# Kernel optimization log

Hardware: AMD Instinct MI355X
Metric: run time of the kernel (lower is better)

Reference implementation:

```python
import jax, jax.numpy as jnp
import numpy as np

N_NODES = 50000
N_EDGES = 800000
D = 128
N_RELS = 460  # 2 * num_rels
N_BASES = 32
SUBMAT = D // N_BASES  # 4
INV_TEMP = 0.1


def setup_inputs() -> dict:
    key = jax.random.key(0)
    ks = jax.random.split(key, 16)
    return {
        "h": jax.random.normal(ks[0], (N_NODES, D), jnp.float32),
        "first_prev": jax.random.normal(ks[1], (N_NODES, D), jnp.float32),
        "second_prev": jax.random.normal(ks[2], (N_NODES, D), jnp.float32),
        "time_diff": jax.random.uniform(ks[3], (N_NODES, 1), jnp.float32),
        "edge_src": jax.random.randint(ks[4], (N_EDGES,), 0, N_NODES, jnp.int32),
        "edge_dst": jax.random.randint(ks[5], (N_EDGES,), 0, N_NODES, jnp.int32),
        "edge_type": jax.random.randint(ks[6], (N_EDGES,), 0, N_RELS, jnp.int32),
        "edge_norm": jax.random.uniform(ks[7], (N_EDGES, 1), jnp.float32),
        "node_norm": jax.random.uniform(ks[8], (N_NODES, 1), jnp.float32),
        "W1": jax.random.normal(ks[9], (N_RELS, N_BASES * SUBMAT * SUBMAT), jnp.float32) * 0.05,
        "W2": jax.random.normal(ks[10], (N_RELS, N_BASES * SUBMAT * SUBMAT), jnp.float32) * 0.05,
        "loop_w1": jax.random.normal(ks[11], (D, D), jnp.float32) * 0.05,
        "loop_w2": jax.random.normal(ks[12], (D, D), jnp.float32) * 0.05,
        "time_w1": jax.random.normal(ks[13], (D, D), jnp.float32) * 0.05,
        "time_w2": jax.random.normal(ks[14], (D, D), jnp.float32) * 0.05,
    }


def _drgcn_layer(h, prev, time_diff, W, loop_w, time_w,
                 edge_src, edge_dst, edge_type, edge_norm, node_norm, activate):
    n = h.shape[0]
    # self-loop message (dropout is identity in eval)
    loop_msg = h @ loop_w                                     # [N, D]
    # block-diagonal per-edge message: gather relation blocks + batched small matmul
    w = W[edge_type].reshape(-1, N_BASES, SUBMAT, SUBMAT)     # [E, B, si, so]
    hs = h[edge_src].reshape(-1, N_BASES, SUBMAT)             # [E, B, si]
    msg = jnp.einsum('ebi,ebio->ebo', hs, w).reshape(-1, h.shape[1])  # [E, D]
    msg = msg * edge_norm                                     # per-edge norm
    agg = jax.ops.segment_sum(msg, edge_dst, num_segments=n)  # scatter-sum to dst
    agg = agg * node_norm                                     # apply_func node norm
    # time-decay residual + self-loop (bias=None in this config)
    out = agg + (prev @ time_w) * jnp.exp(-time_diff * INV_TEMP) + loop_msg
    if activate:
        out = jax.nn.relu(out)
    return out


def reference(h, first_prev, second_prev, time_diff,
              edge_src, edge_dst, edge_type, edge_norm, node_norm,
              W1, W2, loop_w1, loop_w2, time_w1, time_w2):
    h1 = _drgcn_layer(h, first_prev, time_diff, W1, loop_w1, time_w1,
                      edge_src, edge_dst, edge_type, edge_norm, node_norm, activate=False)
    h2 = _drgcn_layer(h1, second_prev, time_diff, W2, loop_w2, time_w2,
                      edge_src, edge_dst, edge_type, edge_norm, node_norm, activate=True)
    return (h1, h2)
```

## Files before the change

### kernel.cpp

```cpp
#include <hip/hip_runtime.h>

#define NN 50000
#define NE 800000
#define DD 128
#define NPAD 50176
#define NBLK_SCAN 196

typedef __attribute__((ext_vector_type(8))) short short8;
typedef __attribute__((ext_vector_type(4))) float f32x4;

static __device__ __forceinline__ float b2f_lo(unsigned u) {
    return __builtin_bit_cast(float, u << 16);
}
static __device__ __forceinline__ float b2f_hi(unsigned u) {
    return __builtin_bit_cast(float, u & 0xffff0000u);
}
static __device__ __forceinline__ unsigned short f2b(float f) {
    unsigned u = __builtin_bit_cast(unsigned, f);
    u += 0x7FFFu + ((u >> 16) & 1u);
    return (unsigned short)(u >> 16);
}
static __device__ __forceinline__ ushort4 f2b4(float4 v) {
    ushort4 u;
    u.x = f2b(v.x); u.y = f2b(v.y); u.z = f2b(v.z); u.w = f2b(v.w);
    return u;
}

__global__ __launch_bounds__(256) void k_hist(
    const int* __restrict__ edst, int* __restrict__ cnt)
{
    const int e = blockIdx.x * 256 + threadIdx.x;
    atomicAdd(&cnt[edst[e]], 1);
}

__global__ __launch_bounds__(256) void k_scan_a(
    const int* __restrict__ cnt, int* __restrict__ bsum)
{
    __shared__ int s[256];
    const int t = threadIdx.x;
    s[t] = cnt[blockIdx.x * 256 + t];
    __syncthreads();
    for (int d = 128; d > 0; d >>= 1) {
        if (t < d) s[t] += s[t + d];
        __syncthreads();
    }
    if (t == 0) bsum[blockIdx.x] = s[0];
}

__global__ __launch_bounds__(256) void k_scan_b(int* __restrict__ bsum)
{
    __shared__ int s[256];
    const int t = threadIdx.x;
    s[t] = (t < NBLK_SCAN) ? bsum[t] : 0;
    __syncthreads();
    for (int d = 1; d < 256; d <<= 1) {
        int v = (t >= d) ? s[t - d] : 0;
        __syncthreads();
        s[t] += v;
        __syncthreads();
    }
    bsum[t] = (t == 0) ? 0 : s[t - 1];
}

__global__ __launch_bounds__(256) void k_scan_c(
    const int* __restrict__ cnt, const int* __restrict__ bsum,
    int* __restrict__ off, int* __restrict__ cur)
{
    __shared__ int s[256];
    const int t = threadIdx.x;
    const int i = blockIdx.x * 256 + t;
    const int c = cnt[i];
    s[t] = c;
    __syncthreads();
    for (int d = 1; d < 256; d <<= 1) {
        int v = (t >= d) ? s[t - d] : 0;
        __syncthreads();
        s[t] += v;
        __syncthreads();
    }
    const int ex = bsum[blockIdx.x] + s[t] - c;
    off[i] = ex;
    cur[i] = ex;
}

__global__ __launch_bounds__(256) void k_scatter(
    const int* __restrict__ esrc, const int* __restrict__ edst,
    const int* __restrict__ etyp, const float* __restrict__ enorm,
    int* __restrict__ cur, int4* __restrict__ sedge)
{
    const int e = blockIdx.x * 256 + threadIdx.x;
    const int d = edst[e];
    const int pos = atomicAdd(&cur[d], 1);
    sedge[pos] = make_int4(esrc[e], etyp[e],
                           __builtin_bit_cast(int, enorm[e]), d);
}

#define PREP_X_BLOCKS 6250
#define PREP_W_BLOCKS 460
#define PREP_BLOCKS   (PREP_X_BLOCKS + PREP_W_BLOCKS + 32)

__global__ __launch_bounds__(256) void k_prep(
    const float* __restrict__ x, const float* __restrict__ fprev,
    const float* __restrict__ sprev, const float* __restrict__ tdiff,
    unsigned short* __restrict__ X1, unsigned short* __restrict__ X2,
    const float* __restrict__ W1, const float* __restrict__ W2,
    unsigned short* __restrict__ W1b, unsigned short* __restrict__ W2b,
    const float* __restrict__ lw1, const float* __restrict__ tw1,
    const float* __restrict__ lw2, const float* __restrict__ tw2,
    unsigned short* __restrict__ Wp1, unsigned short* __restrict__ Wp2)
{
    const int gb = blockIdx.x;
    const int t  = threadIdx.x;
    if (gb < PREP_X_BLOCKS) {
        const int idx = gb * 256 + t;
        const int n = idx >> 5, j = (idx & 31) * 4;
        const float dk = __expf(-tdiff[n] * 0.1f);
        const float4 a = *(const float4*)(x     + (size_t)n * 128 + j);
        float4 b = *(const float4*)(fprev + (size_t)n * 128 + j);
        float4 c = *(const float4*)(sprev + (size_t)n * 128 + j);
        b.x *= dk; b.y *= dk; b.z *= dk; b.w *= dk;
        c.x *= dk; c.y *= dk; c.z *= dk; c.w *= dk;
        *(ushort4*)(X1 + (size_t)n * 256 + j)       = f2b4(a);
        *(ushort4*)(X1 + (size_t)n * 256 + 128 + j) = f2b4(b);
        *(ushort4*)(X2 + (size_t)n * 256 + 128 + j) = f2b4(c);
    } else if (gb < PREP_X_BLOCKS + PREP_W_BLOCKS) {
        const int i = ((gb - PREP_X_BLOCKS) * 256 + t) * 4;
        if (i < 460 * 512) {
            *(ushort4*)(W1b + i) = f2b4(*(const float4*)(W1 + i));
        } else {
            const int k = i - 460 * 512;
            *(ushort4*)(W2b + k) = f2b4(*(const float4*)(W2 + k));
        }
    } else {
        const int g = (gb - PREP_X_BLOCKS - PREP_W_BLOCKS) * 256 + t;
        const int c = g & 4095;
        const float* lw = (g < 4096) ? lw1 : lw2;
        const float* tw = (g < 4096) ? tw1 : tw2;
        unsigned short* Wp = (g < 4096) ? Wp1 : Wp2;
        const int ct = c >> 9, ks = (c >> 6) & 7, lane = c & 63;
        const int col = ct * 16 + (lane & 15);
        unsigned short* o = Wp + (size_t)c * 8;
        #pragma unroll
        for (int i = 0; i < 8; ++i) {
            const int k = ks * 32 + (lane >> 4) * 8 + i;
            const float v = (k < 128) ? lw[(size_t)k * 128 + col]
                                      : tw[(size_t)(k - 128) * 128 + col];
            o[i] = f2b(v);
        }
    }
}

__device__ __forceinline__ void agg_edge(
    const unsigned short* __restrict__ x,
    const unsigned short* __restrict__ Wb,
    const int4* __restrict__ sedge, int i,
    int woff, int l, float4& acc)
{
    const int4 e = sedge[i];
    const int src = __builtin_amdgcn_readfirstlane(e.x);
    const int typ = __builtin_amdgcn_readfirstlane(e.y);
    const float nr = __builtin_bit_cast(float, __builtin_amdgcn_readfirstlane(e.z));
    const unsigned hw = ((const unsigned*)(x + (size_t)src * 256))[l];
    const uint4 wv = *(const uint4*)(Wb + (size_t)typ * 512 + woff);
    const float h0 = b2f_lo(hw) * nr;
    const float h1 = b2f_hi(hw) * nr;
    acc.x += h0 * b2f_lo(wv.x) + h1 * b2f_lo(wv.z);
    acc.y += h0 * b2f_hi(wv.x) + h1 * b2f_hi(wv.z);
    acc.z += h0 * b2f_lo(wv.y) + h1 * b2f_lo(wv.w);
    acc.w += h0 * b2f_hi(wv.y) + h1 * b2f_hi(wv.w);
}

__global__ __launch_bounds__(256) void k_agg2(
    const unsigned short* __restrict__ x,
    const int4*  __restrict__ sedge,
    const int*   __restrict__ off,
    const unsigned short* __restrict__ Wb,
    const float* __restrict__ nnorm,
    float*       __restrict__ agg)
{
    const int l = threadIdx.x & 63;
    const int n = blockIdx.x * 4 + (threadIdx.x >> 6);
    const int beg = off[n], end = off[n + 1];
    const int woff = (l >> 1) * 16 + (l & 1) * 8;

    float4 a0 = {0,0,0,0}, a1 = {0,0,0,0}, a2 = {0,0,0,0}, a3 = {0,0,0,0};

    int i = beg;
    for (; i + 4 <= end; i += 4) {
        agg_edge(x, Wb, sedge, i,     woff, l, a0);
        agg_edge(x, Wb, sedge, i + 1, woff, l, a1);
        agg_edge(x, Wb, sedge, i + 2, woff, l, a2);
        agg_edge(x, Wb, sedge, i + 3, woff, l, a3);
    }
    for (; i < end; ++i) agg_edge(x, Wb, sedge, i, woff, l, a0);

    float4 s;
    s.x = (a0.x + a1.x) + (a2.x + a3.x);
    s.y = (a0.y + a1.y) + (a2.y + a3.y);
    s.z = (a0.z + a1.z) + (a2.z + a3.z);
    s.w = (a0.w + a1.w) + (a2.w + a3.w);
    s.x += __shfl_xor(s.x, 1);
    s.y += __shfl_xor(s.y, 1);
    s.z += __shfl_xor(s.z, 1);
    s.w += __shfl_xor(s.w, 1);

    const float nn = nnorm[n];
    const float e0 = (l & 1) ? s.z : s.x;
    const float e1 = (l & 1) ? s.w : s.y;
    float2* outp = (float2*)(agg + (size_t)n * DD + (l >> 1) * 4 + (l & 1) * 2);
    *outp = make_float2(e0 * nn, e1 * nn);
}

template<int ACT, int WRITE_NEXT>
__global__ __launch_bounds__(256) void combine_mfma(
    const float* __restrict__ agg,
    const unsigned short* __restrict__ X,
    const unsigned short* __restrict__ Wp,
    float* __restrict__ out,
    unsigned short* __restrict__ Xnext)
{
    const int t = threadIdx.x;
    const int l = t & 63;
    const int w = t >> 6;
    const int wr = w >> 1, wc = w & 1;
    const int l15 = l & 15, lhi = l >> 4;
    const int rowbase = blockIdx.x * 64 + wr * 32;

    f32x4 acc[2][4] = {};

    const int ar0 = min(rowbase + l15, NN - 1);
    const int ar1 = min(rowbase + 16 + l15, NN - 1);
    const unsigned short* a0p = X + (size_t)ar0 * 256 + lhi * 8;
    const unsigned short* a1p = X + (size_t)ar1 * 256 + lhi * 8;
    const unsigned short* bp  = Wp + (size_t)(wc * 4) * 8 * 512 + (size_t)l * 8;

    #pragma unroll
    for (int ks = 0; ks < 8; ++ks) {
        const short8 a0 = *(const short8*)(a0p + ks * 32);
        const short8 a1 = *(const short8*)(a1p + ks * 32);
        #pragma unroll
        for (int ct = 0; ct < 4; ++ct) {
            const short8 b = *(const short8*)(bp + (size_t)(ct * 8 + ks) * 512);
            acc[0][ct] = __builtin_amdgcn_mfma_f32_16x16x32_bf16(a0, b, acc[0][ct], 0, 0, 0);
            acc[1][ct] = __builtin_amdgcn_mfma_f32_16x16x32_bf16(a1, b, acc[1][ct], 0, 0, 0);
        }
    }

    __shared__ float cs[64][132];
    #pragma unroll
    for (int rg = 0; rg < 2; ++rg)
        #pragma unroll
        for (int ct = 0; ct < 4; ++ct)
            #pragma unroll
            for (int q = 0; q < 4; ++q)
                cs[wr * 32 + rg * 16 + lhi * 4 + q][wc * 64 + ct * 16 + l15]
                    = acc[rg][ct][q];
    __syncthreads();

    const int r = t >> 2;
    const int s = t & 3;
    const int grow = blockIdx.x * 64 + r;
    if (grow < NN) {
        const float* aggr = agg + (size_t)grow * DD;
        float*       outr = out + (size_t)grow * DD;
        #pragma unroll
        for (int i = 0; i < 8; ++i) {
            const int c = s * 4 + i * 16;
            const float4 a  = *(const float4*)(aggr + c);
            const float4 cc = *(const float4*)&cs[r][c];
            float4 v = make_float4(a.x + cc.x, a.y + cc.y, a.z + cc.z, a.w + cc.w);
            if (ACT) {
                v.x = fmaxf(v.x, 0.f); v.y = fmaxf(v.y, 0.f);
                v.z = fmaxf(v.z, 0.f); v.w = fmaxf(v.w, 0.f);
            }
            *(float4*)(outr + c) = v;
            if (WRITE_NEXT)
                *(ushort4*)(Xnext + (size_t)grow * 256 + c) = f2b4(v);
        }
    }
}

__device__ __forceinline__ float pick4(float4 v, int o) {
    float a = (o & 1) ? v.y : v.x;
    float b = (o & 1) ? v.w : v.z;
    return (o & 2) ? b : a;
}

__global__ __launch_bounds__(256) void k_agg_t2(
    const float* __restrict__ x, const int4* __restrict__ sedge,
    const int* __restrict__ off, const float* __restrict__ W,
    float* __restrict__ agg)
{
    const int lane = threadIdx.x & 63;
    const int n    = blockIdx.x * 4 + (threadIdx.x >> 6);
    const int beg = off[n], end = off[n + 1];
    float4 acca = make_float4(0.f, 0.f, 0.f, 0.f);
    float4 accb = make_float4(0.f, 0.f, 0.f, 0.f);
    for (int i = beg; i < end; ++i) {
        const int4 e = sedge[i];
        const float nr = __builtin_bit_cast(float, e.z);
        const float* wr = W + (size_t)e.y * 512 + 4 * lane;
        const float4 wa = *(const float4*)wr;
        const float4 wb = *(const float4*)(wr + 256);
        const float* hr = x + (size_t)e.x * DD;
        const float ha = hr[lane] * nr;
        const float hb = hr[64 + lane] * nr;
        acca.x += ha * wa.x; acca.y += ha * wa.y; acca.z += ha * wa.z; acca.w += ha * wa.w;
        accb.x += hb * wb.x; accb.y += hb * wb.y; accb.z += hb * wb.z; accb.w += hb * wb.w;
    }
    #pragma unroll
    for (int d = 1; d <= 2; d <<= 1) {
        acca.x += __shfl_xor(acca.x, d); acca.y += __shfl_xor(acca.y, d);
        acca.z += __shfl_xor(acca.z, d); acca.w += __shfl_xor(acca.w, d);
        accb.x += __shfl_xor(accb.x, d); accb.y += __shfl_xor(accb.y, d);
        accb.z += __shfl_xor(accb.z, d); accb.w += __shfl_xor(accb.w, d);
    }
    const int o = lane & 3;
    agg[(size_t)n * DD + lane]      = pick4(acca, o);
    agg[(size_t)n * DD + 64 + lane] = pick4(accb, o);
}

__global__ __launch_bounds__(256) void edge_msg(
    const float* __restrict__ x, const int* __restrict__ esrc,
    const int* __restrict__ edst, const int* __restrict__ etyp,
    const float* __restrict__ enorm, const float* __restrict__ W,
    float* __restrict__ agg)
{
    const int t  = threadIdx.x;
    const int le = t >> 7;
    const int j  = t & 127;
    const int e  = blockIdx.x * 2 + le;
    __shared__ float sh[2][DD];
    sh[le][j] = x[(size_t)esrc[e] * DD + j];
    __syncthreads();
    const int b = j >> 2, o = j & 3;
    const float* wr = W + (size_t)etyp[e] * 512 + b * 16 + o;
    const float4 hv = *(const float4*)&sh[le][b * 4];
    float m = hv.x * wr[0] + hv.y * wr[4] + hv.z * wr[8] + hv.w * wr[12];
    m *= enorm[e];
    atomicAdd(&agg[(size_t)edst[e] * DD + j], m);
}

template<int ACT>
__global__ __launch_bounds__(256) void combine(
    float* __restrict__ out, const float* __restrict__ x,
    const float* __restrict__ prev, const float* __restrict__ tdiff,
    const float* __restrict__ nnorm, const float* __restrict__ lw,
    const float* __restrict__ tw)
{
    const int t = threadIdx.x;
    const int j = t & 127;
    const int r = t >> 7;
    const int base = blockIdx.x * 8;
    __shared__ float sh[8][DD];
    __shared__ float sp[8][DD];
    #pragma unroll
    for (int q = 0; q < 4; ++q) {
        const int m = q * 2 + r;
        const int n = base + m;
        const float decay = __expf(-tdiff[n] * 0.1f);
        sh[m][j] = x[(size_t)n * DD + j];
        sp[m][j] = prev[(size_t)n * DD + j] * decay;
    }
    __syncthreads();
    float acc[4] = {0.f, 0.f, 0.f, 0.f};
    for (int k = 0; k < DD; k += 4) {
        float wl[4], wt[4];
        #pragma unroll
        for (int kk = 0; kk < 4; ++kk) {
            wl[kk] = lw[(size_t)(k + kk) * DD + j];
            wt[kk] = tw[(size_t)(k + kk) * DD + j];
        }
        #pragma unroll
        for (int q = 0; q < 4; ++q) {
            const int m = q * 2 + r;
            const float4 a = *(const float4*)&sh[m][k];
            const float4 p = *(const float4*)&sp[m][k];
            acc[q] += a.x * wl[0] + a.y * wl[1] + a.z * wl[2] + a.w * wl[3]
                    + p.x * wt[0] + p.y * wt[1] + p.z * wt[2] + p.w * wt[3];
        }
    }
    #pragma unroll
    for (int q = 0; q < 4; ++q) {
        const int m = q * 2 + r;
        const int n = base + m;
        float v = out[(size_t)n * DD + j] * nnorm[n] + acc[q];
        if (ACT) v = fmaxf(v, 0.f);
        out[(size_t)n * DD + j] = v;
    }
}

extern "C" void kernel_launch(void* const* d_in, const int* in_sizes, int n_in,
                              void* d_out, int out_size, void* d_ws, size_t ws_size,
                              hipStream_t stream) {
    const float* h     = (const float*)d_in[0];
    const float* fprev = (const float*)d_in[1];
    const float* sprev = (const float*)d_in[2];
    const float* tdiff = (const float*)d_in[3];
    const int*   esrc  = (const int*)d_in[4];
    const int*   edst  = (const int*)d_in[5];
    const int*   etyp  = (const int*)d_in[6];
    const float* enorm = (const float*)d_in[7];
    const float* nnorm = (const float*)d_in[8];
    const float* W1    = (const float*)d_in[9];
    const float* W2    = (const float*)d_in[10];
    const float* lw1   = (const float*)d_in[11];
    const float* lw2   = (const float*)d_in[12];
    const float* tw1   = (const float*)d_in[13];
    const float* tw2   = (const float*)d_in[14];

    float* h1 = (float*)d_out;
    float* h2 = h1 + (size_t)NN * DD;
    const size_t layer_bytes = (size_t)NN * DD * sizeof(float);

    char* wsp = (char*)d_ws;
    int*   cnt   = (int*)wsp;  wsp += (size_t)NPAD * 4;
    int*   off   = (int*)wsp;  wsp += (size_t)NPAD * 4;
    int*   cur   = (int*)wsp;  wsp += (size_t)NPAD * 4;
    int*   bsum  = (int*)wsp;  wsp += 256 * 4;
    int4*  sedge = (int4*)wsp; wsp += (size_t)NE * 16;
    const size_t ws_sorted = (size_t)(wsp - (char*)d_ws);
    unsigned short* X1   = (unsigned short*)wsp; wsp += (size_t)NN * 256 * 2;
    unsigned short* X2   = (unsigned short*)wsp; wsp += (size_t)NN * 256 * 2;
    unsigned short* Wc1p = (unsigned short*)wsp; wsp += 4096 * 8 * 2;
    unsigned short* Wc2p = (unsigned short*)wsp; wsp += 4096 * 8 * 2;
    unsigned short* W1b  = (unsigned short*)wsp; wsp += (size_t)460 * 512 * 2;
    unsigned short* W2b  = (unsigned short*)wsp; wsp += (size_t)460 * 512 * 2;
    const size_t ws_full = (size_t)(wsp - (char*)d_ws);

    const int grid_mm = (NN + 63) / 64;

    if (ws_size >= ws_full) {
        hipMemsetAsync(cnt, 0, (size_t)NPAD * 4, stream);
        k_hist   <<<NE / 256, 256, 0, stream>>>(edst, cnt);
        k_scan_a <<<NBLK_SCAN, 256, 0, stream>>>(cnt, bsum);
        k_scan_b <<<1, 256, 0, stream>>>(bsum);
        k_scan_c <<<NBLK_SCAN, 256, 0, stream>>>(cnt, bsum, off, cur);
        k_scatter<<<NE / 256, 256, 0, stream>>>(esrc, edst, etyp, enorm, cur, sedge);
        k_prep<<<PREP_BLOCKS, 256, 0, stream>>>(
            h, fprev, sprev, tdiff, X1, X2,
            W1, W2, W1b, W2b, lw1, tw1, lw2, tw2, Wc1p, Wc2p);
        k_agg2<<<NN / 4, 256, 0, stream>>>(X1, sedge, off, W1b, nnorm, h1);
        combine_mfma<0, 1><<<grid_mm, 256, 0, stream>>>(h1, X1, Wc1p, h1, X2);
        k_agg2<<<NN / 4, 256, 0, stream>>>(X2, sedge, off, W2b, nnorm, h2);
        combine_mfma<1, 0><<<grid_mm, 256, 0, stream>>>(h2, X2, Wc2p, h2, nullptr);
    } else if (ws_size >= ws_sorted) {
        hipMemsetAsync(cnt, 0, (size_t)NPAD * 4, stream);
        k_hist   <<<NE / 256, 256, 0, stream>>>(edst, cnt);
        k_scan_a <<<NBLK_SCAN, 256, 0, stream>>>(cnt, bsum);
        k_scan_b <<<1, 256, 0, stream>>>(bsum);
        k_scan_c <<<NBLK_SCAN, 256, 0, stream>>>(cnt, bsum, off, cur);
        k_scatter<<<NE / 256, 256, 0, stream>>>(esrc, edst, etyp, enorm, cur, sedge);
        k_agg_t2<<<NN / 4, 256, 0, stream>>>(h, sedge, off, W1, h1);
        combine<0><<<NN / 8, 256, 0, stream>>>(h1, h, fprev, tdiff, nnorm, lw1, tw1);
        k_agg_t2<<<NN / 4, 256, 0, stream>>>(h1, sedge, off, W2, h2);
        combine<1><<<NN / 8, 256, 0, stream>>>(h2, h1, sprev, tdiff, nnorm, lw2, tw2);
    } else {
        hipMemsetAsync(h1, 0, layer_bytes, stream);
        edge_msg<<<NE / 2, 256, 0, stream>>>(h, esrc, edst, etyp, enorm, W1, h1);
        combine<0><<<NN / 8, 256, 0, stream>>>(h1, h, fprev, tdiff, nnorm, lw1, tw1);
        hipMemsetAsync(h2, 0, layer_bytes, stream);
        edge_msg<<<NE / 2, 256, 0, stream>>>(h1, esrc, edst, etyp, enorm, W2, h2);
        combine<1><<<NN / 8, 256, 0, stream>>>(h2, h1, sprev, tdiff, nnorm, lw2, tw2);
    }
}
```

Measured before the change: 423.1 us.

## Fuse CSR build and prep into one cooperative kernel with grid syncs

Replaces the memset, histogram, three scan kernels, scatter and prep launches with a single cooperative kernel of 1024 blocks that separates the phases with grid-wide syncs. The aim is to remove per-launch overhead and gaps between the small kernels that build the destination-sorted edge list. In exchange it adds grid.sync barriers, and 1024 persistent blocks may leave parts of the device idle during the serial scan phases. If the cooperative launch fails, the code falls back to the original sequence of kernels.

```diff
diff --git a/kernel.cpp b/kernel.cpp
--- a/kernel.cpp
+++ b/kernel.cpp
@@ -1,10 +1,14 @@
 #include <hip/hip_runtime.h>
+#include <hip/hip_cooperative_groups.h>
+
+namespace cg = cooperative_groups;
 
 #define NN 50000
 #define NE 800000
 #define DD 128
 #define NPAD 50176
 #define NBLK_SCAN 196
+#define BUILD_BLOCKS 1024
 
 typedef __attribute__((ext_vector_type(8))) short short8;
 typedef __attribute__((ext_vector_type(4))) float f32x4;
@@ -24,6 +28,115 @@
     ushort4 u;
     u.x = f2b(v.x); u.y = f2b(v.y); u.z = f2b(v.z); u.w = f2b(v.w);
     return u;
+}
+
+struct BuildArgs {
+    const int* esrc; const int* edst; const int* etyp; const float* enorm;
+    int* cnt; int* off; int* cur; int* bsum; int4* sedge;
+    const float* x; const float* fprev; const float* sprev; const float* tdiff;
+    unsigned short* X1; unsigned short* X2;
+    const float* W1; const float* W2;
+    unsigned short* W1b; unsigned short* W2b;
+    const float* lw1; const float* tw1; const float* lw2; const float* tw2;
+    unsigned short* Wp1; unsigned short* Wp2;
+};
+
+__global__ __launch_bounds__(256, 4) void k_build(BuildArgs a)
+{
+    cg::grid_group grid = cg::this_grid();
+    const int tid = blockIdx.x * 256 + threadIdx.x;
+    const int nth = gridDim.x * 256;
+
+    for (int i = tid; i < NPAD; i += nth) a.cnt[i] = 0;
+
+    for (int q = tid; q < NN * 32; q += nth) {
+        const int n = q >> 5, j = (q & 31) * 4;
+        const float dk = __expf(-a.tdiff[n] * 0.1f);
+        const float4 xa = *(const float4*)(a.x     + (size_t)n * 128 + j);
+        float4 b = *(const float4*)(a.fprev + (size_t)n * 128 + j);
+        float4 c = *(const float4*)(a.sprev + (size_t)n * 128 + j);
+        b.x *= dk; b.y *= dk; b.z *= dk; b.w *= dk;
+        c.x *= dk; c.y *= dk; c.z *= dk; c.w *= dk;
+        *(ushort4*)(a.X1 + (size_t)n * 256 + j)       = f2b4(xa);
+        *(ushort4*)(a.X1 + (size_t)n * 256 + 128 + j) = f2b4(b);
+        *(ushort4*)(a.X2 + (size_t)n * 256 + 128 + j) = f2b4(c);
+    }
+
+    for (int q = tid; q < 2 * 460 * 512 / 4; q += nth) {
+        const int i = q * 4;
+        if (i < 460 * 512)
+            *(ushort4*)(a.W1b + i) = f2b4(*(const float4*)(a.W1 + i));
+        else {
+            const int k = i - 460 * 512;
+            *(ushort4*)(a.W2b + k) = f2b4(*(const float4*)(a.W2 + k));
+        }
+    }
+
+    for (int g = tid; g < 8192; g += nth) {
+        const int c = g & 4095;
+        const float* lw = (g < 4096) ? a.lw1 : a.lw2;
+        const float* tw = (g < 4096) ? a.tw1 : a.tw2;
+        unsigned short* Wp = (g < 4096) ? a.Wp1 : a.Wp2;
+        const int ct = c >> 9, ks = (c >> 6) & 7, lane = c & 63;
+        const int col = ct * 16 + (lane & 15);
+        unsigned short* o = Wp + (size_t)c * 8;
+        #pragma unroll
+        for (int i = 0; i < 8; ++i) {
+            const int k = ks * 32 + (lane >> 4) * 8 + i;
+            const float v = (k < 128) ? lw[(size_t)k * 128 + col]
+                                      : tw[(size_t)(k - 128) * 128 + col];
+            o[i] = f2b(v);
+        }
+    }
+    grid.sync();
+
+    for (int e = tid; e < NE; e += nth) atomicAdd(&a.cnt[a.edst[e]], 1);
+    grid.sync();
+
+    __shared__ int s[256];
+    if (blockIdx.x < NBLK_SCAN) {
+        const int i = blockIdx.x * 256 + threadIdx.x;
+        const int v = a.cnt[i];
+        s[threadIdx.x] = v;
+        __syncthreads();
+        for (int d = 1; d < 256; d <<= 1) {
+            const int u = (threadIdx.x >= d) ? s[threadIdx.x - d] : 0;
+            __syncthreads();
+            s[threadIdx.x] += u;
+            __syncthreads();
+        }
+        a.off[i] = s[threadIdx.x] - v;
+        if (threadIdx.x == 255) a.bsum[blockIdx.x] = s[255];
+    }
+    grid.sync();
+
+    if (blockIdx.x == 0) {
+        const int v = (threadIdx.x < NBLK_SCAN) ? a.bsum[threadIdx.x] : 0;
+        s[threadIdx.x] = v;
+        __syncthreads();
+        for (int d = 1; d < 256; d <<= 1) {
+            const int u = (threadIdx.x >= d) ? s[threadIdx.x - d] : 0;
+            __syncthreads();
+            s[threadIdx.x] += u;
+            __syncthreads();
+        }
+        a.bsum[threadIdx.x] = s[threadIdx.x] - v;
+    }
+    grid.sync();
+
+    for (int i = tid; i < NPAD; i += nth) {
+        const int o = a.off[i] + a.bsum[i >> 8];
+        a.off[i] = o;
+        a.cur[i] = o;
+    }
+    grid.sync();
+
+    for (int e = tid; e < NE; e += nth) {
+        const int d = a.edst[e];
+        const int pos = atomicAdd(&a.cur[d], 1);
+        a.sedge[pos] = make_int4(a.esrc[e], a.etyp[e],
+                                 __builtin_bit_cast(int, a.enorm[e]), d);
+    }
 }
 
 __global__ __launch_bounds__(256) void k_hist(
@@ -431,15 +544,28 @@
     const int grid_mm = (NN + 63) / 64;
 
     if (ws_size >= ws_full) {
-        hipMemsetAsync(cnt, 0, (size_t)NPAD * 4, stream);
-        k_hist   <<<NE / 256, 256, 0, stream>>>(edst, cnt);
-        k_scan_a <<<NBLK_SCAN, 256, 0, stream>>>(cnt, bsum);
-        k_scan_b <<<1, 256, 0, stream>>>(bsum);
-        k_scan_c <<<NBLK_SCAN, 256, 0, stream>>>(cnt, bsum, off, cur);
-        k_scatter<<<NE / 256, 256, 0, stream>>>(esrc, edst, etyp, enorm, cur, sedge);
-        k_prep<<<PREP_BLOCKS, 256, 0, stream>>>(
-            h, fprev, sprev, tdiff, X1, X2,
-            W1, W2, W1b, W2b, lw1, tw1, lw2, tw2, Wc1p, Wc2p);
+        BuildArgs ba;
+        ba.esrc = esrc; ba.edst = edst; ba.etyp = etyp; ba.enorm = enorm;
+        ba.cnt = cnt; ba.off = off; ba.cur = cur; ba.bsum = bsum; ba.sedge = sedge;
+        ba.x = h; ba.fprev = fprev; ba.sprev = sprev; ba.tdiff = tdiff;
+        ba.X1 = X1; ba.X2 = X2;
+        ba.W1 = W1; ba.W2 = W2; ba.W1b = W1b; ba.W2b = W2b;
+        ba.lw1 = lw1; ba.tw1 = tw1; ba.lw2 = lw2; ba.tw2 = tw2;
+        ba.Wp1 = Wc1p; ba.Wp2 = Wc2p;
+        void* kargs[] = { &ba };
+        hipError_t cerr = hipLaunchCooperativeKernel(
+            (const void*)k_build, dim3(BUILD_BLOCKS), dim3(256), kargs, 0, stream);
+        if (cerr != hipSuccess) {
+            hipMemsetAsync(cnt, 0, (size_t)NPAD * 4, stream);
+            k_hist   <<<NE / 256, 256, 0, stream>>>(edst, cnt);
+            k_scan_a <<<NBLK_SCAN, 256, 0, stream>>>(cnt, bsum);
+            k_scan_b <<<1, 256, 0, stream>>>(bsum);
+            k_scan_c <<<NBLK_SCAN, 256, 0, stream>>>(cnt, bsum, off, cur);
+            k_scatter<<<NE / 256, 256, 0, stream>>>(esrc, edst, etyp, enorm, cur, sedge);
+            k_prep<<<PREP_BLOCKS, 256, 0, stream>>>(
+                h, fprev, sprev, tdiff, X1, X2,
+                W1, W2, W1b, W2b, lw1, tw1, lw2, tw2, Wc1p, Wc2p);
+        }
         k_agg2<<<NN / 4, 256, 0, stream>>>(X1, sedge, off, W1b, nnorm, h1);
         combine_mfma<0, 1><<<grid_mm, 256, 0, stream>>>(h1, X1, Wc1p, h1, X2);
         k_agg2<<<NN / 4, 256, 0, stream>>>(X2, sedge, off, W2b, nnorm, h2);
```

New measurement: 986.7 us. 133% more time.
